# Optimization experiments

Hardware: AMD Instinct MI355X
Metric: run time of the kernel (lower is better)

## Reference

```python
import jax, jax.numpy as jnp
import numpy as np

T, N, E, D, OUT, L = 12, 10000, 160000, 128, 64, 2


def setup_inputs() -> dict:
    key = jax.random.key(0)
    ks = jax.random.split(key, 8)
    s = 1.0 / np.sqrt(D)
    x = jax.random.normal(ks[0], (T, N, D), jnp.float32)
    hidden_states = jax.random.normal(ks[1], (L, N, D), jnp.float32)
    src = jax.random.randint(ks[2], (E,), 0, N, dtype=jnp.int32)
    dst = jax.random.randint(ks[3], (E,), 0, N, dtype=jnp.int32)
    W_self = jax.random.normal(ks[4], (L, 6, D, D), jnp.float32) * s
    W_neigh = jax.random.normal(ks[5], (L, 6, D, D), jnp.float32) * s
    b = jnp.zeros((L, 6, D), jnp.float32)
    W_out = jax.random.normal(ks[6], (D, OUT), jnp.float32) * s
    b_out = jnp.zeros((OUT,), jnp.float32)
    return dict(x=x, hidden_states=hidden_states, W_self=W_self, W_neigh=W_neigh,
                b=b, W_out=W_out, b_out=b_out, src=src, dst=dst)


def reference(x, hidden_states, W_self, W_neigh, b, W_out, b_out, src, dst):
    n_nodes = x.shape[1]
    deg = jax.ops.segment_sum(jnp.ones_like(dst, jnp.float32), dst, num_segments=n_nodes)
    deg_inv = jnp.where(deg > 0, 1.0 / deg, 0.0)[:, None]  # [N,1]

    def agg(f):  # mean over in-neighbors (DGL update_all copy_u + mean)
        return jax.ops.segment_sum(f[src], dst, num_segments=n_nodes) * deg_inv

    # agg_seq=True: original concatenates all timesteps and does one update_all;
    # mean is per-feature, so this equals per-timestep neighbor means, vmapped.
    hN_all = jax.vmap(agg)(x)  # [T,N,D]

    def net(f, fN, i, Ws, Wn, bl):  # SAGE-mean style message-passing net
        return f @ Ws[i] + fN @ Wn[i] + bl[i]

    def cell(xin, h, hN_x, Ws, Wn, bl):
        if hN_x is None:
            hN_x = agg(xin)
        hN_h = agg(h)
        r = jax.nn.sigmoid(net(xin, hN_x, 0, Ws, Wn, bl) + net(h, hN_h, 1, Ws, Wn, bl))
        u = jax.nn.sigmoid(net(xin, hN_x, 2, Ws, Wn, bl) + net(h, hN_h, 3, Ws, Wn, bl))
        c = jnp.tanh(net(xin, hN_x, 4, Ws, Wn, bl) + net(h, hN_h, 5, Ws, Wn, bl))
        return u * h + (1.0 - u) * c  # note: r*h is dead code in the source

    def step(hidden, inp_t):
        x_t, hN_t = inp_t
        cur, hN = x_t, hN_t
        new_h = []
        for j in range(L):  # small fixed depth
            cur = cell(cur, hidden[j], hN, W_self[j], W_neigh[j], b[j])
            new_h.append(cur)
            hN = None  # h_N only used by first layer (as in source)
        out = cur @ W_out + b_out
        return jnp.stack(new_h), out

    hidden_final, outputs = jax.lax.scan(step, hidden_states, (x, hN_all))
    return outputs, hidden_final
```

## Files before the change

### kernel.cpp

```cpp
#include <hip/hip_runtime.h>

typedef unsigned short u16;
typedef unsigned int   u32;
typedef __attribute__((ext_vector_type(4))) float f32x4;
typedef __attribute__((ext_vector_type(8))) short s16x8;

#define TT 12
#define NN 10000
#define EE 160000
#define DD 128
#define OO 64

__device__ __forceinline__ u16 f2bf(float f) {
  union { float f; u32 u; } x; x.f = f;
  u32 r = x.u + 0x7FFFu + ((x.u >> 16) & 1u);
  return (u16)(r >> 16);
}
__device__ __forceinline__ float bf2f(u16 v) {
  union { u32 u; float f; } x; x.u = (u32)v << 16; return x.f;
}

__global__ __launch_bounds__(256) void count_kernel(const int* __restrict__ dst,
                                                    int* __restrict__ deg, int E) {
  int e = blockIdx.x * 256 + threadIdx.x;
  if (e < E) atomicAdd(&deg[dst[e]], 1);
}

__global__ __launch_bounds__(1024) void scan_kernel(const int* __restrict__ deg,
                                                    int* __restrict__ offs,
                                                    float* __restrict__ dinv, int n) {
  __shared__ int buf[1024];
  __shared__ int carry_s;
  int tid = threadIdx.x;
  if (tid == 0) carry_s = 0;
  __syncthreads();
  for (int base = 0; base < n; base += 1024) {
    int v = (base + tid < n) ? deg[base + tid] : 0;
    buf[tid] = v;
    __syncthreads();
    for (int off = 1; off < 1024; off <<= 1) {
      int t = (tid >= off) ? buf[tid - off] : 0;
      __syncthreads();
      buf[tid] += t;
      __syncthreads();
    }
    int carry = carry_s;
    if (base + tid < n) {
      offs[base + tid] = carry + buf[tid] - v;
      dinv[base + tid] = (v > 0) ? 1.0f / (float)v : 0.0f;
    }
    __syncthreads();
    if (tid == 1023) carry_s = carry + buf[1023];
    __syncthreads();
  }
  if (tid == 0) offs[n] = carry_s;
}

__global__ __launch_bounds__(256) void fill_kernel(const int* __restrict__ src,
                                                   const int* __restrict__ dst,
                                                   const int* __restrict__ offs,
                                                   int* __restrict__ cursor,
                                                   int* __restrict__ csr, int E) {
  int e = blockIdx.x * 256 + threadIdx.x;
  if (e >= E) return;
  int d = dst[e];
  int pos = atomicAdd(&cursor[d], 1);
  csr[offs[d] + pos] = src[e];
}

__global__ __launch_bounds__(256) void pack_kernel(const float* __restrict__ Wself,
                                                   const float* __restrict__ Wneigh,
                                                   const float* __restrict__ b,
                                                   const float* __restrict__ Wout,
                                                   u16* __restrict__ Wp,
                                                   float* __restrict__ biasbuf,
                                                   u16* __restrict__ WoT) {
  int gid = blockIdx.x * 256 + threadIdx.x;
  const int NWP = 2 * 256 * 512;
  if (gid < NWP) {
    int j = gid >> 17;
    int rem = gid & 131071;
    int c = rem >> 9;
    int k = rem & 511;
    int seg = k >> 7, kd = k & 127;
    int cc = c & 127;
    int gate = (c < 128) ? (seg < 2 ? 2 : 3) : (seg < 2 ? 4 : 5);
    const float* M = (seg & 1) ? Wneigh : Wself;
    float v = M[((j * 6 + gate) * 128 + kd) * 128 + cc];
    Wp[gid] = f2bf(v);
  } else if (gid < NWP + 64 * 128) {
    int i = gid - NWP;
    int c = i >> 7, k = i & 127;
    WoT[i] = f2bf(Wout[k * OO + c]);
  } else if (gid < NWP + 64 * 128 + 512) {
    int i = gid - NWP - 64 * 128;
    int j = i >> 8, g = (i >> 7) & 1, d = i & 127;
    int g1 = g ? 4 : 2, g2 = g ? 5 : 3;
    biasbuf[i] = b[(j * 6 + g1) * 128 + d] + b[(j * 6 + g2) * 128 + d];
  }
}

__global__ __launch_bounds__(256) void cvt_kernel(const float* __restrict__ x,
                                                  const float* __restrict__ hs,
                                                  u16* __restrict__ xb,
                                                  float* __restrict__ h0f,
                                                  u16* __restrict__ hb0,
                                                  float* __restrict__ h1f,
                                                  u16* __restrict__ hb1,
                                                  int nx4, int nh4half) {
  int i = blockIdx.x * 256 + threadIdx.x;
  if (i < nx4) {
    float4 v = *(const float4*)(x + (size_t)i * 4);
    uint2 p;
    p.x = (u32)f2bf(v.x) | ((u32)f2bf(v.y) << 16);
    p.y = (u32)f2bf(v.z) | ((u32)f2bf(v.w) << 16);
    *(uint2*)(xb + (size_t)i * 4) = p;
  } else if (i < nx4 + 2 * nh4half) {
    int j = i - nx4;
    int half = (j >= nh4half);
    int jj = half ? j - nh4half : j;
    float4 v = ((const float4*)hs)[j];
    float* fdst = half ? h1f : h0f;
    u16*   bdst = half ? hb1 : hb0;
    ((float4*)fdst)[jj] = v;
    uint2 p;
    p.x = (u32)f2bf(v.x) | ((u32)f2bf(v.y) << 16);
    p.y = (u32)f2bf(v.z) | ((u32)f2bf(v.w) << 16);
    ((uint2*)bdst)[jj] = p;
  }
}

__device__ __forceinline__ void agg_one(const int* __restrict__ offs,
                                        const int* __restrict__ csr,
                                        const float* __restrict__ dinv,
                                        const u32* __restrict__ S,
                                        u32* __restrict__ O,
                                        int node, int lane) {
  int nu = __builtin_amdgcn_readfirstlane(node);
  int e0 = offs[nu], e1 = offs[nu + 1];
  float di = dinv[nu];
  float xa = 0.f, ya = 0.f, xb_ = 0.f, yb_ = 0.f;
  int e = e0;
  for (; e + 4 <= e1; e += 4) {
    int i0 = csr[e], i1 = csr[e + 1], i2 = csr[e + 2], i3 = csr[e + 3];
    u32 v0 = S[i0 * 64 + lane];
    u32 v1 = S[i1 * 64 + lane];
    u32 v2 = S[i2 * 64 + lane];
    u32 v3 = S[i3 * 64 + lane];
    xa  += bf2f((u16)v0) + bf2f((u16)v1);
    ya  += bf2f((u16)(v0 >> 16)) + bf2f((u16)(v1 >> 16));
    xb_ += bf2f((u16)v2) + bf2f((u16)v3);
    yb_ += bf2f((u16)(v2 >> 16)) + bf2f((u16)(v3 >> 16));
  }
  for (; e < e1; ++e) {
    u32 v = S[csr[e] * 64 + lane];
    xa += bf2f((u16)v); ya += bf2f((u16)(v >> 16));
  }
  float sx = (xa + xb_) * di, sy = (ya + yb_) * di;
  O[nu * 64 + lane] = (u32)f2bf(sx) | ((u32)f2bf(sy) << 16);
}

__global__ __launch_bounds__(256) void aggs_kernel(const int* __restrict__ offs,
                                                   const int* __restrict__ csr,
                                                   const float* __restrict__ dinv,
                                                   const u16* __restrict__ s,
                                                   u16* __restrict__ o, int N) {
  int node = blockIdx.x * 4 + (threadIdx.x >> 6);
  if (node >= N) return;
  size_t yo = (size_t)blockIdx.y * N * 64;
  agg_one(offs, csr, dinv, (const u32*)s + yo, (u32*)o + yo, node, threadIdx.x & 63);
}

__global__ __launch_bounds__(256) void aggdual_kernel(const int* __restrict__ offs,
                                                      const int* __restrict__ csr,
                                                      const float* __restrict__ dinv,
                                                      const u16* __restrict__ s0,
                                                      const u16* __restrict__ s1,
                                                      u16* __restrict__ o0,
                                                      u16* __restrict__ o1, int N) {
  int b = blockIdx.x;
  int srcsel = (b >> 2) & 1;
  int idx = (b >> 3) * 4 + (b & 3);
  int node = idx * 4 + (threadIdx.x >> 6);
  if (node >= N) return;
  const u32* S = (const u32*)(srcsel ? s1 : s0);
  u32* O = (u32*)(srcsel ? o1 : o0);
  agg_one(offs, csr, dinv, S, O, node, threadIdx.x & 63);
}

template <int MODE>
__device__ __forceinline__ void cell_body(char* __restrict__ smem, int row0, int tid,
    const u16* __restrict__ s0, const u16* __restrict__ s1,
    const u16* __restrict__ s2, const u16* __restrict__ s3,
    const u16* __restrict__ W, const float* __restrict__ bias,
    float* __restrict__ P,
    const float* __restrict__ hin, float* __restrict__ hout, u16* __restrict__ hbout,
    const u16* __restrict__ WoT, const float* __restrict__ bout,
    float* __restrict__ outp, int N) {
  constexpr int NKC = (MODE == 2) ? 8 : 4;
  u16* As = (u16*)smem;
  u16* Bs = (u16*)(smem + 8192);
  const u16* srcs[4] = {s0, s1, s2, s3};
  int lane = tid & 63, w = tid >> 6;
  int wr = w & 3, wc = w >> 2;

  f32x4 accU[4], accC[4];
  if constexpr (MODE == 1) {
    #pragma unroll
    for (int n = 0; n < 4; ++n) {
      int col = wc * 64 + n * 16 + (lane & 15);
      #pragma unroll
      for (int r = 0; r < 4; ++r) {
        int row = row0 + wr * 16 + (lane >> 4) * 4 + r;
        accU[n][r] = (row < N) ? P[(size_t)row * 256 + col] : 0.f;
        accC[n][r] = (row < N) ? P[(size_t)row * 256 + col + 128] : 0.f;
      }
    }
  } else {
    #pragma unroll
    for (int n = 0; n < 4; ++n) { accU[n] = (f32x4){0,0,0,0}; accC[n] = (f32x4){0,0,0,0}; }
  }

  #pragma unroll
  for (int kc = 0; kc < NKC; ++kc) {
    {
      int r = tid >> 3, k8 = (tid & 7) * 8;
      const u16* sp = srcs[kc >> 1];
      int grow = row0 + r;
      uint4 v = make_uint4(0, 0, 0, 0);
      if (grow < N) v = *(const uint4*)(sp + (size_t)grow * DD + (kc & 1) * 64 + k8);
      int byte = (r * 128 + (tid & 7) * 16) ^ ((r & 7) << 4);
      *(uint4*)((char*)As + byte) = v;
    }
    #pragma unroll
    for (int it = 0; it < 4; ++it) {
      int id = it * 512 + tid;
      int c = id >> 3, k8 = (id & 7) * 8;
      uint4 v = *(const uint4*)(W + c * 512 + kc * 64 + k8);
      int byte = (c * 128 + (id & 7) * 16) ^ ((c & 7) << 4);
      *(uint4*)((char*)Bs + byte) = v;
    }
    __syncthreads();
    #pragma unroll
    for (int ks = 0; ks < 2; ++ks) {
      int arow = wr * 16 + (lane & 15);
      int abyte = (arow * 128 + ks * 64 + (lane >> 4) * 16) ^ ((arow & 7) << 4);
      s16x8 af = *(const s16x8*)((char*)As + abyte);
      #pragma unroll
      for (int n = 0; n < 4; ++n) {
        int cu = wc * 64 + n * 16 + (lane & 15);
        int bub = (cu * 128 + ks * 64 + (lane >> 4) * 16) ^ ((cu & 7) << 4);
        s16x8 bu = *(const s16x8*)((char*)Bs + bub);
        accU[n] = __builtin_amdgcn_mfma_f32_16x16x32_bf16(af, bu, accU[n], 0, 0, 0);
        int cc = cu + 128;
        int bcb = (cc * 128 + ks * 64 + (lane >> 4) * 16) ^ ((cc & 7) << 4);
        s16x8 bc = *(const s16x8*)((char*)Bs + bcb);
        accC[n] = __builtin_amdgcn_mfma_f32_16x16x32_bf16(af, bc, accC[n], 0, 0, 0);
      }
    }
    __syncthreads();
  }

  if constexpr (MODE == 0) {
    #pragma unroll
    for (int n = 0; n < 4; ++n) {
      int col = wc * 64 + n * 16 + (lane & 15);
      #pragma unroll
      for (int r = 0; r < 4; ++r) {
        int row = row0 + wr * 16 + (lane >> 4) * 4 + r;
        if (row < N) {
          P[(size_t)row * 256 + col] = accU[n][r];
          P[(size_t)row * 256 + col + 128] = accC[n][r];
        }
      }
    }
  } else {
    #pragma unroll
    for (int n = 0; n < 4; ++n) {
      int col = wc * 64 + n * 16 + (lane & 15);
      float bu = bias[col], bc = bias[128 + col];
      #pragma unroll
      for (int r = 0; r < 4; ++r) {
        int row = row0 + wr * 16 + (lane >> 4) * 4 + r;
        if (row < N) {
          float u = 1.0f / (1.0f + __expf(-(accU[n][r] + bu)));
          float cg = tanhf(accC[n][r] + bc);
          size_t idx = (size_t)row * DD + col;
          float hn = u * hin[idx] + (1.0f - u) * cg;
          hout[idx] = hn;
          u16 hnb = f2bf(hn);
          hbout[idx] = hnb;
          if constexpr (MODE == 2) {
            int rl = row - row0;
            int hbyte = (rl * 256 + col * 2) ^ ((rl & 7) << 4);
            *(u16*)(smem + hbyte) = hnb;
          }
        }
      }
    }
    if constexpr (MODE == 2) {
      #pragma unroll
      for (int it = 0; it < 2; ++it) {
        int id = it * 512 + tid;
        int c = id >> 4, kc8 = (id & 15) * 8;
        uint4 v = *(const uint4*)(WoT + c * 128 + kc8);
        int byte = (c * 256 + kc8 * 2) ^ ((c & 7) << 4);
        *(uint4*)(smem + 16384 + byte) = v;
      }
      __syncthreads();
      f32x4 ao[2] = {};
      #pragma unroll
      for (int ks = 0; ks < 4; ++ks) {
        int arow = wr * 16 + (lane & 15);
        int abyte = (arow * 256 + ks * 64 + (lane >> 4) * 16) ^ ((arow & 7) << 4);
        s16x8 af = *(const s16x8*)(smem + abyte);
        #pragma unroll
        for (int n = 0; n < 2; ++n) {
          int co = wc * 32 + n * 16 + (lane & 15);
          int bbyte = (co * 256 + ks * 64 + (lane >> 4) * 16) ^ ((co & 7) << 4);
          s16x8 bf = *(const s16x8*)(smem + 16384 + bbyte);
          ao[n] = __builtin_amdgcn_mfma_f32_16x16x32_bf16(af, bf, ao[n], 0, 0, 0);
        }
      }
      #pragma unroll
      for (int n = 0; n < 2; ++n) {
        int co = wc * 32 + n * 16 + (lane & 15);
        float bb = bout[co];
        #pragma unroll
        for (int r = 0; r < 4; ++r) {
          int row = row0 + wr * 16 + (lane >> 4) * 4 + r;
          if (row < N) outp[(size_t)row * OO + co] = ao[n][r] + bb;
        }
      }
    }
  }
}

__global__ __launch_bounds__(512) void pre_kernel(const u16* __restrict__ xb,
                                                  const u16* __restrict__ axb,
                                                  const u16* __restrict__ Wp,
                                                  float* __restrict__ P, int N) {
  __shared__ __align__(16) char smem[40960];
  size_t yo = (size_t)blockIdx.y * N * DD;
  cell_body<0>(smem, blockIdx.x * 64, threadIdx.x, xb + yo, axb + yo, nullptr, nullptr,
               Wp, nullptr, P + (size_t)blockIdx.y * N * 256,
               nullptr, nullptr, nullptr, nullptr, nullptr, nullptr, N);
}

__global__ __launch_bounds__(512) void cell0_kernel(const u16* __restrict__ hb0c,
                                                    const u16* __restrict__ ah0,
                                                    const u16* __restrict__ W,
                                                    const float* __restrict__ bias,
                                                    float* __restrict__ Pt,
                                                    const float* __restrict__ h0in,
                                                    float* __restrict__ h0out,
                                                    u16* __restrict__ hb0out, int N) {
  __shared__ __align__(16) char smem[40960];
  cell_body<1>(smem, blockIdx.x * 64, threadIdx.x, hb0c, ah0, nullptr, nullptr,
               W, bias, Pt, h0in, h0out, hb0out, nullptr, nullptr, nullptr, N);
}

template <int WITHC0>
__global__ __launch_bounds__(512) void step_kernel(const u16* __restrict__ hb0c,
                                                   const u16* __restrict__ ah0,
                                                   const u16* __restrict__ hb1r,
                                                   const u16* __restrict__ ah1,
                                                   const u16* __restrict__ Wp,
                                                   const float* __restrict__ biasbuf,
                                                   float* __restrict__ Pn,
                                                   float* __restrict__ h1f,
                                                   u16* __restrict__ hb1w,
                                                   const float* __restrict__ h0in,
                                                   float* __restrict__ h0out,
                                                   u16* __restrict__ hb0out,
                                                   const u16* __restrict__ WoT,
                                                   const float* __restrict__ bout,
                                                   float* __restrict__ outp, int N) {
  __shared__ __align__(16) char smem[40960];
  int bx = blockIdx.x;
  int role = WITHC0 ? (bx & 1) : 0;
  int row0 = (WITHC0 ? (bx >> 1) : bx) * 64;
  if (role == 0) {
    cell_body<2>(smem, row0, threadIdx.x, hb0c, ah0, hb1r, ah1,
                 Wp + 131072, biasbuf + 256, nullptr,
                 h1f, h1f, hb1w, WoT, bout, outp, N);
  } else {
    cell_body<1>(smem, row0, threadIdx.x, hb0c, ah0, nullptr, nullptr,
                 Wp + 256, biasbuf, Pn,
                 h0in, h0out, hb0out, nullptr, nullptr, nullptr, N);
  }
}

extern "C" void kernel_launch(void* const* d_in, const int* in_sizes, int n_in,
                              void* d_out, int out_size, void* d_ws, size_t ws_size,
                              hipStream_t stream) {
  const float* x      = (const float*)d_in[0];
  const float* hs     = (const float*)d_in[1];
  const float* Wself  = (const float*)d_in[2];
  const float* Wneigh = (const float*)d_in[3];
  const float* b      = (const float*)d_in[4];
  const float* Wout   = (const float*)d_in[5];
  const float* bout   = (const float*)d_in[6];
  const int*   src    = (const int*)d_in[7];
  const int*   dst    = (const int*)d_in[8];
  float* out = (float*)d_out;

  const int N = NN, E = EE, D = DD, T = TT;

  char* ws = (char*)d_ws;
  size_t off = 0;
  auto alloc = [&](size_t bytes) -> void* {
    void* p = ws + off;
    off = (off + bytes + 255) & ~(size_t)255;
    return p;
  };
  int*   deg     = (int*)alloc(N * 4);
  int*   offs    = (int*)alloc((N + 1) * 4);
  int*   cursor  = (int*)alloc(N * 4);
  int*   csr     = (int*)alloc(E * 4);
  float* dinv    = (float*)alloc(N * 4);
  u16*   Wp      = (u16*)alloc(2 * 256 * 512 * 2);
  float* biasbuf = (float*)alloc(512 * 4);
  u16*   WoT     = (u16*)alloc(64 * 128 * 2);
  float* h0A     = (float*)alloc((size_t)N * D * 4);
  float* h0B     = (float*)alloc((size_t)N * D * 4);
  float* h1f     = (float*)alloc((size_t)N * D * 4);
  u16*   hb0A    = (u16*)alloc((size_t)N * D * 2);
  u16*   hb0B    = (u16*)alloc((size_t)N * D * 2);
  u16*   hb1     = (u16*)alloc((size_t)N * D * 2);
  u16*   ah0b    = (u16*)alloc((size_t)N * D * 2);
  u16*   ah1b    = (u16*)alloc((size_t)N * D * 2);
  u16*   xb      = (u16*)alloc((size_t)T * N * D * 2);
  u16*   axb     = (u16*)alloc((size_t)T * N * D * 2);
  float* P       = (float*)alloc((size_t)T * N * 256 * 4);

  float* h0f[2] = {h0A, h0B};
  u16*   hb0[2] = {hb0A, hb0B};

  hipMemsetAsync(deg, 0, N * 4, stream);
  hipMemsetAsync(cursor, 0, N * 4, stream);
  count_kernel<<<(E + 255) / 256, 256, 0, stream>>>(dst, deg, E);
  scan_kernel<<<1, 1024, 0, stream>>>(deg, offs, dinv, N);
  fill_kernel<<<(E + 255) / 256, 256, 0, stream>>>(src, dst, offs, cursor, csr, E);
  {
    int tot = 2 * 256 * 512 + 64 * 128 + 512;
    pack_kernel<<<(tot + 255) / 256, 256, 0, stream>>>(Wself, Wneigh, b, Wout, Wp, biasbuf, WoT);
  }
  {
    int nx4 = T * N * D / 4, nh4half = N * D / 4;
    cvt_kernel<<<(nx4 + 2 * nh4half + 255) / 256, 256, 0, stream>>>(
        x, hs, xb, h0A, hb0A, h1f, hb1, nx4, nh4half);
  }

  int aggGrid = (N + 3) / 4;
  int mmGrid  = (N + 63) / 64;

  aggs_kernel<<<dim3(aggGrid, T), 256, 0, stream>>>(offs, csr, dinv, xb, axb, N);
  pre_kernel<<<dim3(mmGrid, T), 512, 0, stream>>>(xb, axb, Wp, P, N);
  aggs_kernel<<<aggGrid, 256, 0, stream>>>(offs, csr, dinv, hb0A, ah0b, N);
  cell0_kernel<<<mmGrid, 512, 0, stream>>>(hb0A, ah0b, Wp + 256, biasbuf, P,
                                           h0A, h0B, hb0B, N);

  for (int t = 0; t < T; ++t) {
    u16* cur = hb0[(t + 1) & 1];
    aggdual_kernel<<<2 * aggGrid, 256, 0, stream>>>(offs, csr, dinv, cur, hb1,
                                                    ah0b, ah1b, N);
    if (t < T - 1) {
      step_kernel<1><<<2 * mmGrid, 512, 0, stream>>>(
          cur, ah0b, hb1, ah1b, Wp, biasbuf,
          P + (size_t)(t + 1) * N * 256,
          h1f, hb1,
          h0f[(t + 1) & 1], h0f[t & 1], hb0[t & 1],
          WoT, bout, out + (size_t)t * N * OO, N);
    } else {
      step_kernel<0><<<mmGrid, 512, 0, stream>>>(
          cur, ah0b, hb1, ah1b, Wp, biasbuf, nullptr,
          h1f, hb1, nullptr, nullptr, nullptr,
          WoT, bout, out + (size_t)t * N * OO, N);
    }
  }
  hipMemcpyAsync(out + (size_t)T * N * OO, h0f[0], (size_t)N * D * 4,
                 hipMemcpyDeviceToDevice, stream);
  hipMemcpyAsync(out + (size_t)T * N * OO + (size_t)N * D, h1f, (size_t)N * D * 4,
                 hipMemcpyDeviceToDevice, stream);
}
```

Before: 735.9 us.

## Fuse prep kernels, faster scan, premultiplied CSR, wider gather unroll, direct final writes

Merges the degree count, weight packing and input conversion into a single prep launch. Replaces the serial block scan with a one-pass LDS and wave-shuffle scan, and stores CSR indices premultiplied by the row stride. The neighbor gather loop is unrolled to 8 edges with more accumulators, and the x aggregation is reordered across timesteps for cache locality. Final hidden states are written straight into the output, removing two device copies. These changes cut launch and copy overhead and raise memory-level parallelism in the gathers, at the cost of more registers and a scan that assumes N fits in 10240.

```diff
diff --git a/kernel.cpp b/kernel.cpp
--- a/kernel.cpp
+++ b/kernel.cpp
@@ -20,103 +20,28 @@
   union { u32 u; float f; } x; x.u = (u32)v << 16; return x.f;
 }
 
-__global__ __launch_bounds__(256) void count_kernel(const int* __restrict__ dst,
-                                                    int* __restrict__ deg, int E) {
-  int e = blockIdx.x * 256 + threadIdx.x;
-  if (e < E) atomicAdd(&deg[dst[e]], 1);
-}
-
-__global__ __launch_bounds__(1024) void scan_kernel(const int* __restrict__ deg,
-                                                    int* __restrict__ offs,
-                                                    float* __restrict__ dinv, int n) {
-  __shared__ int buf[1024];
-  __shared__ int carry_s;
-  int tid = threadIdx.x;
-  if (tid == 0) carry_s = 0;
-  __syncthreads();
-  for (int base = 0; base < n; base += 1024) {
-    int v = (base + tid < n) ? deg[base + tid] : 0;
-    buf[tid] = v;
-    __syncthreads();
-    for (int off = 1; off < 1024; off <<= 1) {
-      int t = (tid >= off) ? buf[tid - off] : 0;
-      __syncthreads();
-      buf[tid] += t;
-      __syncthreads();
-    }
-    int carry = carry_s;
-    if (base + tid < n) {
-      offs[base + tid] = carry + buf[tid] - v;
-      dinv[base + tid] = (v > 0) ? 1.0f / (float)v : 0.0f;
-    }
-    __syncthreads();
-    if (tid == 1023) carry_s = carry + buf[1023];
-    __syncthreads();
-  }
-  if (tid == 0) offs[n] = carry_s;
-}
-
-__global__ __launch_bounds__(256) void fill_kernel(const int* __restrict__ src,
-                                                   const int* __restrict__ dst,
-                                                   const int* __restrict__ offs,
-                                                   int* __restrict__ cursor,
-                                                   int* __restrict__ csr, int E) {
-  int e = blockIdx.x * 256 + threadIdx.x;
-  if (e >= E) return;
-  int d = dst[e];
-  int pos = atomicAdd(&cursor[d], 1);
-  csr[offs[d] + pos] = src[e];
-}
-
-__global__ __launch_bounds__(256) void pack_kernel(const float* __restrict__ Wself,
-                                                   const float* __restrict__ Wneigh,
-                                                   const float* __restrict__ b,
-                                                   const float* __restrict__ Wout,
-                                                   u16* __restrict__ Wp,
-                                                   float* __restrict__ biasbuf,
-                                                   u16* __restrict__ WoT) {
+__global__ __launch_bounds__(256) void prep_kernel(
+    const float* __restrict__ x, const float* __restrict__ hs,
+    const int* __restrict__ dst,
+    const float* __restrict__ Wself, const float* __restrict__ Wneigh,
+    const float* __restrict__ b, const float* __restrict__ Wout,
+    u16* __restrict__ xb, float* __restrict__ h0f, u16* __restrict__ hb0,
+    float* __restrict__ h1f, u16* __restrict__ hb1,
+    int* __restrict__ deg, u16* __restrict__ Wp,
+    float* __restrict__ biasbuf, u16* __restrict__ WoT,
+    int nx4, int nh4half, int E) {
   int gid = blockIdx.x * 256 + threadIdx.x;
   const int NWP = 2 * 256 * 512;
-  if (gid < NWP) {
-    int j = gid >> 17;
-    int rem = gid & 131071;
-    int c = rem >> 9;
-    int k = rem & 511;
-    int seg = k >> 7, kd = k & 127;
-    int cc = c & 127;
-    int gate = (c < 128) ? (seg < 2 ? 2 : 3) : (seg < 2 ? 4 : 5);
-    const float* M = (seg & 1) ? Wneigh : Wself;
-    float v = M[((j * 6 + gate) * 128 + kd) * 128 + cc];
-    Wp[gid] = f2bf(v);
-  } else if (gid < NWP + 64 * 128) {
-    int i = gid - NWP;
-    int c = i >> 7, k = i & 127;
-    WoT[i] = f2bf(Wout[k * OO + c]);
-  } else if (gid < NWP + 64 * 128 + 512) {
-    int i = gid - NWP - 64 * 128;
-    int j = i >> 8, g = (i >> 7) & 1, d = i & 127;
-    int g1 = g ? 4 : 2, g2 = g ? 5 : 3;
-    biasbuf[i] = b[(j * 6 + g1) * 128 + d] + b[(j * 6 + g2) * 128 + d];
-  }
-}
-
-__global__ __launch_bounds__(256) void cvt_kernel(const float* __restrict__ x,
-                                                  const float* __restrict__ hs,
-                                                  u16* __restrict__ xb,
-                                                  float* __restrict__ h0f,
-                                                  u16* __restrict__ hb0,
-                                                  float* __restrict__ h1f,
-                                                  u16* __restrict__ hb1,
-                                                  int nx4, int nh4half) {
-  int i = blockIdx.x * 256 + threadIdx.x;
-  if (i < nx4) {
-    float4 v = *(const float4*)(x + (size_t)i * 4);
+  int cvtEnd  = nx4 + 2 * nh4half;
+  int cntEnd  = cvtEnd + E;
+  if (gid < nx4) {
+    float4 v = *(const float4*)(x + (size_t)gid * 4);
     uint2 p;
     p.x = (u32)f2bf(v.x) | ((u32)f2bf(v.y) << 16);
     p.y = (u32)f2bf(v.z) | ((u32)f2bf(v.w) << 16);
-    *(uint2*)(xb + (size_t)i * 4) = p;
-  } else if (i < nx4 + 2 * nh4half) {
-    int j = i - nx4;
+    *(uint2*)(xb + (size_t)gid * 4) = p;
+  } else if (gid < cvtEnd) {
+    int j = gid - nx4;
     int half = (j >= nh4half);
     int jj = half ? j - nh4half : j;
     float4 v = ((const float4*)hs)[j];
@@ -127,7 +52,83 @@
     p.x = (u32)f2bf(v.x) | ((u32)f2bf(v.y) << 16);
     p.y = (u32)f2bf(v.z) | ((u32)f2bf(v.w) << 16);
     ((uint2*)bdst)[jj] = p;
-  }
+  } else if (gid < cntEnd) {
+    int e = gid - cvtEnd;
+    atomicAdd(&deg[dst[e]], 1);
+  } else {
+    int pg = gid - cntEnd;
+    if (pg < NWP) {
+      int j = pg >> 17;
+      int rem = pg & 131071;
+      int c = rem >> 9;
+      int k = rem & 511;
+      int seg = k >> 7, kd = k & 127;
+      int cc = c & 127;
+      int gate = (c < 128) ? (seg < 2 ? 2 : 3) : (seg < 2 ? 4 : 5);
+      const float* M = (seg & 1) ? Wneigh : Wself;
+      float v = M[((j * 6 + gate) * 128 + kd) * 128 + cc];
+      Wp[pg] = f2bf(v);
+    } else if (pg < NWP + 64 * 128) {
+      int i = pg - NWP;
+      int c = i >> 7, k = i & 127;
+      WoT[i] = f2bf(Wout[k * OO + c]);
+    } else if (pg < NWP + 64 * 128 + 512) {
+      int i = pg - NWP - 64 * 128;
+      int j = i >> 8, g = (i >> 7) & 1, d = i & 127;
+      int g1 = g ? 4 : 2, g2 = g ? 5 : 3;
+      biasbuf[i] = b[(j * 6 + g1) * 128 + d] + b[(j * 6 + g2) * 128 + d];
+    }
+  }
+}
+
+__global__ __launch_bounds__(1024) void scan_kernel(const int* __restrict__ deg,
+                                                    int* __restrict__ offs,
+                                                    float* __restrict__ dinv, int n) {
+  __shared__ int lds_deg[10240];
+  __shared__ int wsum[16];
+  int tid = threadIdx.x;
+  for (int i = tid; i < 10240; i += 1024) lds_deg[i] = (i < n) ? deg[i] : 0;
+  __syncthreads();
+  int base = tid * 10;
+  int loc[10];
+  int s = 0;
+  #pragma unroll
+  for (int k = 0; k < 10; ++k) { loc[k] = s; s += lds_deg[base + k]; }
+  int lane = tid & 63;
+  int incl = s;
+  #pragma unroll
+  for (int d = 1; d < 64; d <<= 1) {
+    int t2 = __shfl_up(incl, d);
+    if (lane >= d) incl += t2;
+  }
+  int wid = tid >> 6;
+  if (lane == 63) wsum[wid] = incl;
+  __syncthreads();
+  int wpre = 0;
+  for (int k = 0; k < wid; ++k) wpre += wsum[k];
+  int excl = wpre + incl - s;
+  #pragma unroll
+  for (int k = 0; k < 10; ++k) {
+    int idx = base + k;
+    if (idx < n) {
+      int d0 = lds_deg[idx];
+      offs[idx] = excl + loc[k];
+      dinv[idx] = (d0 > 0) ? 1.0f / (float)d0 : 0.0f;
+    }
+  }
+  if (tid == 1023) offs[n] = excl + s;
+}
+
+__global__ __launch_bounds__(256) void fill_kernel(const int* __restrict__ src,
+                                                   const int* __restrict__ dst,
+                                                   const int* __restrict__ offs,
+                                                   int* __restrict__ cursor,
+                                                   int* __restrict__ csr, int E) {
+  int e = blockIdx.x * 256 + threadIdx.x;
+  if (e >= E) return;
+  int d = dst[e];
+  int pos = atomicAdd(&cursor[d], 1);
+  csr[offs[d] + pos] = src[e] * 64;
 }
 
 __device__ __forceinline__ void agg_one(const int* __restrict__ offs,
@@ -140,23 +141,36 @@
   int e0 = offs[nu], e1 = offs[nu + 1];
   float di = dinv[nu];
   float xa = 0.f, ya = 0.f, xb_ = 0.f, yb_ = 0.f;
+  float xc = 0.f, yc = 0.f, xd = 0.f, yd = 0.f;
   int e = e0;
-  for (; e + 4 <= e1; e += 4) {
-    int i0 = csr[e], i1 = csr[e + 1], i2 = csr[e + 2], i3 = csr[e + 3];
-    u32 v0 = S[i0 * 64 + lane];
-    u32 v1 = S[i1 * 64 + lane];
-    u32 v2 = S[i2 * 64 + lane];
-    u32 v3 = S[i3 * 64 + lane];
+  for (; e + 8 <= e1; e += 8) {
+    int i0 = csr[e],     i1 = csr[e + 1], i2 = csr[e + 2], i3 = csr[e + 3];
+    int i4 = csr[e + 4], i5 = csr[e + 5], i6 = csr[e + 6], i7 = csr[e + 7];
+    u32 v0 = S[i0 + lane], v1 = S[i1 + lane], v2 = S[i2 + lane], v3 = S[i3 + lane];
+    u32 v4 = S[i4 + lane], v5 = S[i5 + lane], v6 = S[i6 + lane], v7 = S[i7 + lane];
     xa  += bf2f((u16)v0) + bf2f((u16)v1);
     ya  += bf2f((u16)(v0 >> 16)) + bf2f((u16)(v1 >> 16));
     xb_ += bf2f((u16)v2) + bf2f((u16)v3);
     yb_ += bf2f((u16)(v2 >> 16)) + bf2f((u16)(v3 >> 16));
+    xc  += bf2f((u16)v4) + bf2f((u16)v5);
+    yc  += bf2f((u16)(v4 >> 16)) + bf2f((u16)(v5 >> 16));
+    xd  += bf2f((u16)v6) + bf2f((u16)v7);
+    yd  += bf2f((u16)(v6 >> 16)) + bf2f((u16)(v7 >> 16));
+  }
+  for (; e + 4 <= e1; e += 4) {
+    int i0 = csr[e], i1 = csr[e + 1], i2 = csr[e + 2], i3 = csr[e + 3];
+    u32 v0 = S[i0 + lane], v1 = S[i1 + lane], v2 = S[i2 + lane], v3 = S[i3 + lane];
+    xa  += bf2f((u16)v0) + bf2f((u16)v1);
+    ya  += bf2f((u16)(v0 >> 16)) + bf2f((u16)(v1 >> 16));
+    xb_ += bf2f((u16)v2) + bf2f((u16)v3);
+    yb_ += bf2f((u16)(v2 >> 16)) + bf2f((u16)(v3 >> 16));
   }
   for (; e < e1; ++e) {
-    u32 v = S[csr[e] * 64 + lane];
+    u32 v = S[csr[e] + lane];
     xa += bf2f((u16)v); ya += bf2f((u16)(v >> 16));
   }
-  float sx = (xa + xb_) * di, sy = (ya + yb_) * di;
+  float sx = ((xa + xb_) + (xc + xd)) * di;
+  float sy = ((ya + yb_) + (yc + yd)) * di;
   O[nu * 64 + lane] = (u32)f2bf(sx) | ((u32)f2bf(sy) << 16);
 }
 
@@ -167,8 +181,29 @@
                                                    u16* __restrict__ o, int N) {
   int node = blockIdx.x * 4 + (threadIdx.x >> 6);
   if (node >= N) return;
-  size_t yo = (size_t)blockIdx.y * N * 64;
-  agg_one(offs, csr, dinv, (const u32*)s + yo, (u32*)o + yo, node, threadIdx.x & 63);
+  agg_one(offs, csr, dinv, (const u32*)s, (u32*)o, node, threadIdx.x & 63);
+}
+
+__global__ __launch_bounds__(256) void aggx_kernel(const int* __restrict__ offs,
+                                                   const int* __restrict__ csr,
+                                                   const float* __restrict__ dinv,
+                                                   const u16* __restrict__ xb,
+                                                   u16* __restrict__ axb, int N) {
+  int id = blockIdx.x;
+  int t, grp;
+  if (id < 20000) {
+    t = id & 7;
+    grp = id >> 3;
+  } else {
+    int j = id - 20000;
+    int slot = j & 7;
+    t = 8 + (slot & 3);
+    grp = (slot >> 2) * 1250 + (j >> 3);
+  }
+  int node = grp * 4 + (threadIdx.x >> 6);
+  if (node >= N) return;
+  size_t yo = (size_t)t * N * 64;
+  agg_one(offs, csr, dinv, (const u32*)xb + yo, (u32*)axb + yo, node, threadIdx.x & 63);
 }
 
 __global__ __launch_bounds__(256) void aggdual_kernel(const int* __restrict__ offs,
@@ -368,7 +403,8 @@
                                                    const u16* __restrict__ Wp,
                                                    const float* __restrict__ biasbuf,
                                                    float* __restrict__ Pn,
-                                                   float* __restrict__ h1f,
+                                                   const float* __restrict__ h1in,
+                                                   float* __restrict__ h1out,
                                                    u16* __restrict__ hb1w,
                                                    const float* __restrict__ h0in,
                                                    float* __restrict__ h0out,
@@ -383,7 +419,7 @@
   if (role == 0) {
     cell_body<2>(smem, row0, threadIdx.x, hb0c, ah0, hb1r, ah1,
                  Wp + 131072, biasbuf + 256, nullptr,
-                 h1f, h1f, hb1w, WoT, bout, outp, N);
+                 h1in, h1out, hb1w, WoT, bout, outp, N);
   } else {
     cell_body<1>(smem, row0, threadIdx.x, hb0c, ah0, nullptr, nullptr,
                  Wp + 256, biasbuf, Pn,
@@ -436,26 +472,25 @@
 
   float* h0f[2] = {h0A, h0B};
   u16*   hb0[2] = {hb0A, hb0B};
+  float* hid0 = out + (size_t)T * N * OO;
+  float* hid1 = hid0 + (size_t)N * D;
 
   hipMemsetAsync(deg, 0, N * 4, stream);
   hipMemsetAsync(cursor, 0, N * 4, stream);
-  count_kernel<<<(E + 255) / 256, 256, 0, stream>>>(dst, deg, E);
+  {
+    int nx4 = T * N * D / 4, nh4half = N * D / 4;
+    int tot = nx4 + 2 * nh4half + E + (2 * 256 * 512 + 64 * 128 + 512);
+    prep_kernel<<<(tot + 255) / 256, 256, 0, stream>>>(
+        x, hs, dst, Wself, Wneigh, b, Wout,
+        xb, h0A, hb0A, h1f, hb1, deg, Wp, biasbuf, WoT, nx4, nh4half, E);
+  }
   scan_kernel<<<1, 1024, 0, stream>>>(deg, offs, dinv, N);
   fill_kernel<<<(E + 255) / 256, 256, 0, stream>>>(src, dst, offs, cursor, csr, E);
-  {
-    int tot = 2 * 256 * 512 + 64 * 128 + 512;
-    pack_kernel<<<(tot + 255) / 256, 256, 0, stream>>>(Wself, Wneigh, b, Wout, Wp, biasbuf, WoT);
-  }
-  {
-    int nx4 = T * N * D / 4, nh4half = N * D / 4;
-    cvt_kernel<<<(nx4 + 2 * nh4half + 255) / 256, 256, 0, stream>>>(
-        x, hs, xb, h0A, hb0A, h1f, hb1, nx4, nh4half);
-  }
 
   int aggGrid = (N + 3) / 4;
   int mmGrid  = (N + 63) / 64;
 
-  aggs_kernel<<<dim3(aggGrid, T), 256, 0, stream>>>(offs, csr, dinv, xb, axb, N);
+  aggx_kernel<<<30000, 256, 0, stream>>>(offs, csr, dinv, xb, axb, N);
   pre_kernel<<<dim3(mmGrid, T), 512, 0, stream>>>(xb, axb, Wp, P, N);
   aggs_kernel<<<aggGrid, 256, 0, stream>>>(offs, csr, dinv, hb0A, ah0b, N);
   cell0_kernel<<<mmGrid, 512, 0, stream>>>(hb0A, ah0b, Wp + 256, biasbuf, P,
@@ -466,21 +501,18 @@
     aggdual_kernel<<<2 * aggGrid, 256, 0, stream>>>(offs, csr, dinv, cur, hb1,
                                                     ah0b, ah1b, N);
     if (t < T - 1) {
+      float* h0o = (t == T - 2) ? hid0 : h0f[t & 1];
       step_kernel<1><<<2 * mmGrid, 512, 0, stream>>>(
           cur, ah0b, hb1, ah1b, Wp, biasbuf,
           P + (size_t)(t + 1) * N * 256,
-          h1f, hb1,
-          h0f[(t + 1) & 1], h0f[t & 1], hb0[t & 1],
+          h1f, h1f, hb1,
+          h0f[(t + 1) & 1], h0o, hb0[t & 1],
           WoT, bout, out + (size_t)t * N * OO, N);
     } else {
       step_kernel<0><<<mmGrid, 512, 0, stream>>>(
           cur, ah0b, hb1, ah1b, Wp, biasbuf, nullptr,
-          h1f, hb1, nullptr, nullptr, nullptr,
+          h1f, hid1, hb1, nullptr, nullptr, nullptr,
           WoT, bout, out + (size_t)t * N * OO, N);
     }
   }
-  hipMemcpyAsync(out + (size_t)T * N * OO, h0f[0], (size_t)N * D * 4,
-                 hipMemcpyDeviceToDevice, stream);
-  hipMemcpyAsync(out + (size_t)T * N * OO + (size_t)N * D, h1f, (size_t)N * D * 4,
-                 hipMemcpyDeviceToDevice, stream);
-}
+}
```

Result: faster. 681.0 us (-7.5%).
